# Performance work log

Hardware: AMD Instinct MI355X
Metric: run time of the kernel (lower is better)

Reference implementation:

```python
import jax, jax.numpy as jnp
import numpy as np

B, C, W, H, D = 2, 256, 32, 32, 32
CH = C // 2  # 128
LN_EPS = 1e-5


def _spatial_pool(x, wm, bm):
    # x: [B,C,W,H,D]; wm: [C]; bm: scalar. 1x1x1 conv C->1 == channel dot.
    b, c = x.shape[0], x.shape[1]
    xf = x.reshape(b, c, -1)                       # [B,C,N]
    mask = jnp.einsum('bcn,c->bn', xf, wm) + bm    # [B,N]
    attn = jax.nn.softmax(mask, axis=1)            # softmax over spatial N
    return jnp.einsum('bcn,bn->bc', xf, attn)      # [B,C] weighted-sum pool


def _channel_add(ctx, w1, b1, g, be, w2, b2):
    # 1x1 conv C->C/2, LayerNorm over C/2, ReLU, 1x1 conv C/2->C
    h = ctx @ w1.T + b1                            # [B,CH]
    mu = jnp.mean(h, axis=-1, keepdims=True)
    var = jnp.mean((h - mu) ** 2, axis=-1, keepdims=True)
    h = (h - mu) * jax.lax.rsqrt(var + LN_EPS) * g + be
    h = jax.nn.relu(h)
    return h @ w2.T + b2                           # [B,C]


def setup_inputs() -> dict:
    key = jax.random.key(0)
    ks = jax.random.split(key, 20)
    s = 0.02
    d = {
        'preds_S': jax.random.normal(ks[0], (B, C, W, H, D), jnp.float32),
        'preds_T': jax.random.normal(ks[1], (B, C, W, H, D), jnp.float32),
        'wm_s': jax.random.normal(ks[2], (C,), jnp.float32) * s,
        'bm_s': jnp.zeros((), jnp.float32),
        'wm_t': jax.random.normal(ks[3], (C,), jnp.float32) * s,
        'bm_t': jnp.zeros((), jnp.float32),
        'w1_s': jax.random.normal(ks[4], (CH, C), jnp.float32) * s,
        'b1_s': jnp.zeros((CH,), jnp.float32),
        'g_s': jnp.ones((CH,), jnp.float32),
        'be_s': jnp.zeros((CH,), jnp.float32),
        'w2_s': jax.random.normal(ks[5], (C, CH), jnp.float32) * s,
        'b2_s': jnp.zeros((C,), jnp.float32),
        'w1_t': jax.random.normal(ks[6], (CH, C), jnp.float32) * s,
        'b1_t': jnp.zeros((CH,), jnp.float32),
        'g_t': jnp.ones((CH,), jnp.float32),
        'be_t': jnp.zeros((CH,), jnp.float32),
        'w2_t': jax.random.normal(ks[7], (C, CH), jnp.float32) * s,
        'b2_t': jnp.zeros((C,), jnp.float32),
    }
    return d


def reference(preds_S, preds_T, wm_s, bm_s, wm_t, bm_t,
              w1_s, b1_s, g_s, be_s, w2_s, b2_s,
              w1_t, b1_t, g_t, be_t, w2_t, b2_t):
    ctx_s = _spatial_pool(preds_S, wm_s, bm_s)     # [B,C]
    ctx_t = _spatial_pool(preds_T, wm_t, bm_t)
    add_s = _channel_add(ctx_s, w1_s, b1_s, g_s, be_s, w2_s, b2_s)  # [B,C]
    add_t = _channel_add(ctx_t, w1_t, b1_t, g_t, be_t, w2_t, b2_t)
    out_s = preds_S + add_s[:, :, None, None, None]
    out_t = preds_T + add_t[:, :, None, None, None]
    diff = out_s - out_t
    return jnp.sum(diff * diff) / preds_S.shape[0]
```

## Files before the change

### kernel.cpp

```cpp
#include <hip/hip_runtime.h>
#include <math.h>

#define Bc   2
#define Cc   256
#define Nn   32768
#define CHc  128
#define LN_EPS 1e-5f

#define TN    64
#define TPB   512
#define NQ    16
#define CG    32
#define CPG   8
#define GRIDX (Nn / TN)

__global__ __launch_bounds__(TPB, 2) void gc_fused(
    const float* __restrict__ S, const float* __restrict__ T,
    const float* __restrict__ wms, const float* __restrict__ bms,
    const float* __restrict__ wmt, const float* __restrict__ bmt,
    float* __restrict__ ctxnum,
    float* __restrict__ rowsum,
    float* __restrict__ den,
    float* __restrict__ sumsq) {
  const int b    = blockIdx.y;
  const int tid  = threadIdx.x;
  const int nq   = tid & (NQ - 1);
  const int cg   = tid >> 4;
  const int wv   = tid >> 6;
  const int lane = tid & 63;
  const int c0   = cg * CPG;
  const int n0   = blockIdx.x * TN + nq * 4;

  __shared__ float4 mredw[2][8][NQ];
  __shared__ float  cred[Cc * 17];
  __shared__ float  sqred[8];
  __shared__ float  denred[2][NQ];

  const float bS = bms[0];
  const float bT = bmt[0];

  const float* Sp = S + ((size_t)b * Cc + c0) * Nn + n0;
  const float* Tp = T + ((size_t)b * Cc + c0) * Nn + n0;

  float4 s4[CPG], t4[CPG];
#pragma unroll
  for (int i = 0; i < CPG; ++i) s4[i] = *(const float4*)(Sp + (size_t)i * Nn);
#pragma unroll
  for (int i = 0; i < CPG; ++i) t4[i] = *(const float4*)(Tp + (size_t)i * Nn);

  float wS[CPG], wT[CPG];
#pragma unroll
  for (int i = 0; i < CPG; ++i) { wS[i] = wms[c0 + i]; wT[i] = wmt[c0 + i]; }

  float4 ms = make_float4(0.f, 0.f, 0.f, 0.f);
  float4 mt = make_float4(0.f, 0.f, 0.f, 0.f);
#pragma unroll
  for (int i = 0; i < CPG; ++i) {
    ms.x += wS[i] * s4[i].x; ms.y += wS[i] * s4[i].y;
    ms.z += wS[i] * s4[i].z; ms.w += wS[i] * s4[i].w;
    mt.x += wT[i] * t4[i].x; mt.y += wT[i] * t4[i].y;
    mt.z += wT[i] * t4[i].z; mt.w += wT[i] * t4[i].w;
  }

#pragma unroll
  for (int m = 16; m <= 32; m <<= 1) {
    ms.x += __shfl_xor(ms.x, m); ms.y += __shfl_xor(ms.y, m);
    ms.z += __shfl_xor(ms.z, m); ms.w += __shfl_xor(ms.w, m);
    mt.x += __shfl_xor(mt.x, m); mt.y += __shfl_xor(mt.y, m);
    mt.z += __shfl_xor(mt.z, m); mt.w += __shfl_xor(mt.w, m);
  }
  if (lane < NQ) { mredw[0][wv][nq] = ms; mredw[1][wv][nq] = mt; }

  __syncthreads();

  float4 Ms = make_float4(0.f, 0.f, 0.f, 0.f);
  float4 Mt = make_float4(0.f, 0.f, 0.f, 0.f);
#pragma unroll
  for (int w = 0; w < 8; ++w) {
    const float4 a = mredw[0][w][nq];
    Ms.x += a.x; Ms.y += a.y; Ms.z += a.z; Ms.w += a.w;
    const float4 c = mredw[1][w][nq];
    Mt.x += c.x; Mt.y += c.y; Mt.z += c.z; Mt.w += c.w;
  }
  float4 es, et;
  es.x = __expf(Ms.x + bS); es.y = __expf(Ms.y + bS);
  es.z = __expf(Ms.z + bS); es.w = __expf(Ms.w + bS);
  et.x = __expf(Mt.x + bT); et.y = __expf(Mt.y + bT);
  et.z = __expf(Mt.z + bT); et.w = __expf(Mt.w + bT);

  if (tid < NQ) {
    denred[0][tid] = es.x + es.y + es.z + es.w;
    denred[1][tid] = et.x + et.y + et.z + et.w;
  }

#pragma unroll
  for (int i = 0; i < CPG; ++i)
    cred[(c0 + i) * 17 + nq] =
        s4[i].x * es.x + s4[i].y * es.y + s4[i].z * es.z + s4[i].w * es.w;
  __syncthreads();
  if (tid < Cc) {
    float a = 0.f;
#pragma unroll
    for (int k = 0; k < NQ; ++k) a += cred[tid * 17 + k];
    atomicAdd(&ctxnum[((size_t)0 * Bc + b) * Cc + tid], a);
  } else if (tid == Cc + 1) {
    float a = 0.f, c = 0.f;
#pragma unroll
    for (int k = 0; k < NQ; ++k) { a += denred[0][k]; c += denred[1][k]; }
    atomicAdd(&den[0 * Bc + b], a);
    atomicAdd(&den[1 * Bc + b], c);
  }
  __syncthreads();

#pragma unroll
  for (int i = 0; i < CPG; ++i)
    cred[(c0 + i) * 17 + nq] =
        t4[i].x * et.x + t4[i].y * et.y + t4[i].z * et.z + t4[i].w * et.w;
  __syncthreads();
  if (tid < Cc) {
    float c = 0.f;
#pragma unroll
    for (int k = 0; k < NQ; ++k) c += cred[tid * 17 + k];
    atomicAdd(&ctxnum[((size_t)1 * Bc + b) * Cc + tid], c);
  }
  __syncthreads();

  float sq = 0.f;
#pragma unroll
  for (int i = 0; i < CPG; ++i) {
    const float dx = s4[i].x - t4[i].x, dy = s4[i].y - t4[i].y;
    const float dz = s4[i].z - t4[i].z, dw = s4[i].w - t4[i].w;
    cred[(c0 + i) * 17 + nq] = dx + dy + dz + dw;
    sq += dx * dx + dy * dy + dz * dz + dw * dw;
  }
#pragma unroll
  for (int m = 1; m < 64; m <<= 1) sq += __shfl_xor(sq, m);
  if (lane == 0) sqred[wv] = sq;
  __syncthreads();
  if (tid < Cc) {
    float r = 0.f;
#pragma unroll
    for (int k = 0; k < NQ; ++k) r += cred[tid * 17 + k];
    atomicAdd(&rowsum[(size_t)b * Cc + tid], r);
  } else if (tid == Cc) {
    float v = 0.f;
#pragma unroll
    for (int w = 0; w < 8; ++w) v += sqred[w];
    atomicAdd(sumsq, v);
  }
}

__global__ __launch_bounds__(1024) void gc_k4a_mlp(
    const float* __restrict__ ctxr, const float* __restrict__ den,
    const float* __restrict__ w1s, const float* __restrict__ b1s,
    const float* __restrict__ gs,  const float* __restrict__ bes,
    const float* __restrict__ w2s, const float* __restrict__ b2s,
    const float* __restrict__ w1t, const float* __restrict__ b1t,
    const float* __restrict__ gt,  const float* __restrict__ bet,
    const float* __restrict__ w2t, const float* __restrict__ b2t,
    float* __restrict__ addv) {
  const int tt  = blockIdx.x >> 1;
  const int b   = blockIdx.x & 1;
  const int tid = threadIdx.x;

  const float* w1 = tt ? w1t : w1s;
  const float* b1 = tt ? b1t : b1s;
  const float* g  = tt ? gt  : gs;
  const float* be = tt ? bet : bes;
  const float* w2 = tt ? w2t : w2s;
  const float* b2 = tt ? b2t : b2s;

  __shared__ float cxs[Cc];
  __shared__ float part[1024];
  __shared__ float hbuf[CHc];
  __shared__ float hr[CHc];
  __shared__ float2 red2[128];
  __shared__ float mu_s, rstd_s;

  if (tid < Cc)
    cxs[tid] = ctxr[((size_t)tt * Bc + b) * Cc + tid] / den[tt * Bc + b];
  __syncthreads();

  {
    const int j = tid >> 3, s = tid & 7;
    const float* wr = w1 + j * Cc + s * 32;
    const float4* cx4 = (const float4*)(cxs + s * 32);
    float acc = 0.f;
#pragma unroll
    for (int k = 0; k < 8; ++k) {
      const float4 w = *(const float4*)(wr + k * 4);
      const float4 x = cx4[k];
      acc += w.x * x.x + w.y * x.y + w.z * x.z + w.w * x.w;
    }
    part[tid] = acc;
  }
  __syncthreads();
  if (tid < CHc) {
    float h = b1[tid];
#pragma unroll
    for (int q = 0; q < 8; ++q) h += part[tid * 8 + q];
    hbuf[tid] = h;
  }
  __syncthreads();

  if (tid < CHc) {
    const float v = hbuf[tid];
    red2[tid] = make_float2(v, v * v);
  }
  __syncthreads();
  for (int s = 64; s > 0; s >>= 1) {
    if (tid < s) {
      red2[tid].x += red2[tid + s].x;
      red2[tid].y += red2[tid + s].y;
    }
    __syncthreads();
  }
  if (tid == 0) {
    const float mu = red2[0].x / (float)CHc;
    const float var = red2[0].y / (float)CHc - mu * mu;
    mu_s = mu;
    rstd_s = rsqrtf(var + LN_EPS);
  }
  __syncthreads();
  if (tid < CHc) {
    const float v = (hbuf[tid] - mu_s) * rstd_s * g[tid] + be[tid];
    hr[tid] = v > 0.f ? v : 0.f;
  }
  __syncthreads();

  {
    const int c = tid >> 2, q = tid & 3;
    const float* wr = w2 + c * CHc + q * 32;
    const float4* h4 = (const float4*)(hr + q * 32);
    float acc = 0.f;
#pragma unroll
    for (int k = 0; k < 8; ++k) {
      const float4 w = *(const float4*)(wr + k * 4);
      const float4 x = h4[k];
      acc += w.x * x.x + w.y * x.y + w.z * x.z + w.w * x.w;
    }
    part[tid] = acc;
  }
  __syncthreads();
  if (tid < Cc) {
    float acc = b2[tid];
#pragma unroll
    for (int q = 0; q < 4; ++q) acc += part[tid * 4 + q];
    addv[((size_t)tt * Bc + b) * Cc + tid] = acc;
  }
}

__global__ __launch_bounds__(256) void gc_k4b_final(
    const float* __restrict__ addv, const float* __restrict__ rowsum,
    const float* __restrict__ sumsq, float* __restrict__ out) {
  const int tid = threadIdx.x;
  __shared__ float red[256];
  float part = 0.f;
  for (int job = tid; job < Bc * Cc; job += 256) {
    const int c = job & (Cc - 1);
    const int b = job >> 8;
    const float delta = addv[((size_t)0 * Bc + b) * Cc + c] -
                        addv[((size_t)1 * Bc + b) * Cc + c];
    part += 2.f * delta * rowsum[(size_t)b * Cc + c] +
            (float)Nn * delta * delta;
  }
  red[tid] = part;
  __syncthreads();
  for (int s = 128; s > 0; s >>= 1) {
    if (tid < s) red[tid] += red[tid + s];
    __syncthreads();
  }
  if (tid == 0) out[0] = (red[0] + sumsq[0]) / (float)Bc;
}

extern "C" void kernel_launch(void* const* d_in, const int* in_sizes, int n_in,
                              void* d_out, int out_size, void* d_ws,
                              size_t ws_size, hipStream_t stream) {
  const float* S   = (const float*)d_in[0];
  const float* T   = (const float*)d_in[1];
  const float* wms = (const float*)d_in[2];
  const float* bms = (const float*)d_in[3];
  const float* wmt = (const float*)d_in[4];
  const float* bmt = (const float*)d_in[5];
  const float* w1s = (const float*)d_in[6];
  const float* b1s = (const float*)d_in[7];
  const float* gs  = (const float*)d_in[8];
  const float* bes = (const float*)d_in[9];
  const float* w2s = (const float*)d_in[10];
  const float* b2s = (const float*)d_in[11];
  const float* w1t = (const float*)d_in[12];
  const float* b1t = (const float*)d_in[13];
  const float* gt  = (const float*)d_in[14];
  const float* bet = (const float*)d_in[15];
  const float* w2t = (const float*)d_in[16];
  const float* b2t = (const float*)d_in[17];
  float* out = (float*)d_out;

  float* ws     = (float*)d_ws;
  float* ctxnum = ws;
  float* rowsum = ctxnum + 2 * Bc * Cc;
  float* den    = rowsum + Bc * Cc;
  float* sumsq  = den + 4;
  float* addv   = sumsq + 1;

  hipMemsetAsync(d_ws, 0, (2 * Bc * Cc + Bc * Cc + 4 + 1) * sizeof(float),
                 stream);

  gc_fused<<<dim3(GRIDX, Bc), TPB, 0, stream>>>(S, T, wms, bms, wmt, bmt,
                                                ctxnum, rowsum, den, sumsq);
  gc_k4a_mlp<<<4, 1024, 0, stream>>>(ctxnum, den, w1s, b1s, gs, bes, w2s, b2s,
                                     w1t, b1t, gt, bet, w2t, b2t, addv);
  gc_k4b_final<<<1, 256, 0, stream>>>(addv, rowsum, sumsq, out);
}
```

Before: 205.8 us.

## Merge shared-memory reductions into one barrier and fuse final kernel via last-block atomic

The fused streaming kernel gets three separate shared-memory scratch arrays, one each for the S-weighted, T-weighted and difference partials. This replaces four barrier-separated reduction phases with a single barrier, and the work is split so the upper 256 threads reduce the T context in parallel with the lower 256. Empty asm constraints pin the loaded S/T values in registers. The final scalar reduction kernel is folded into the MLP kernel through a last-block-done atomic counter, removing one launch. In exchange, shared memory rises from about 17KB to about 52KB per block, which may lower occupancy at two blocks per CU.

```diff
diff --git a/kernel.cpp b/kernel.cpp
--- a/kernel.cpp
+++ b/kernel.cpp
@@ -32,7 +32,9 @@
   const int n0   = blockIdx.x * TN + nq * 4;
 
   __shared__ float4 mredw[2][8][NQ];
-  __shared__ float  cred[Cc * 17];
+  __shared__ float  creds[Cc * 17];
+  __shared__ float  credt[Cc * 17];
+  __shared__ float  credd[Cc * 17];
   __shared__ float  sqred[8];
   __shared__ float  denred[2][NQ];
 
@@ -63,6 +65,14 @@
   }
 
 #pragma unroll
+  for (int i = 0; i < CPG; ++i) {
+    asm volatile("" : "+v"(s4[i].x), "+v"(s4[i].y), "+v"(s4[i].z),
+                      "+v"(s4[i].w));
+    asm volatile("" : "+v"(t4[i].x), "+v"(t4[i].y), "+v"(t4[i].z),
+                      "+v"(t4[i].w));
+  }
+
+#pragma unroll
   for (int m = 16; m <= 32; m <<= 1) {
     ms.x += __shfl_xor(ms.x, m); ms.y += __shfl_xor(ms.y, m);
     ms.z += __shfl_xor(ms.z, m); ms.w += __shfl_xor(ms.w, m);
@@ -95,62 +105,57 @@
 
 #pragma unroll
   for (int i = 0; i < CPG; ++i)
-    cred[(c0 + i) * 17 + nq] =
+    creds[(c0 + i) * 17 + nq] =
         s4[i].x * es.x + s4[i].y * es.y + s4[i].z * es.z + s4[i].w * es.w;
-  __syncthreads();
-  if (tid < Cc) {
-    float a = 0.f;
-#pragma unroll
-    for (int k = 0; k < NQ; ++k) a += cred[tid * 17 + k];
-    atomicAdd(&ctxnum[((size_t)0 * Bc + b) * Cc + tid], a);
-  } else if (tid == Cc + 1) {
-    float a = 0.f, c = 0.f;
-#pragma unroll
-    for (int k = 0; k < NQ; ++k) { a += denred[0][k]; c += denred[1][k]; }
-    atomicAdd(&den[0 * Bc + b], a);
-    atomicAdd(&den[1 * Bc + b], c);
-  }
-  __syncthreads();
-
 #pragma unroll
   for (int i = 0; i < CPG; ++i)
-    cred[(c0 + i) * 17 + nq] =
+    credt[(c0 + i) * 17 + nq] =
         t4[i].x * et.x + t4[i].y * et.y + t4[i].z * et.z + t4[i].w * et.w;
-  __syncthreads();
-  if (tid < Cc) {
-    float c = 0.f;
-#pragma unroll
-    for (int k = 0; k < NQ; ++k) c += cred[tid * 17 + k];
-    atomicAdd(&ctxnum[((size_t)1 * Bc + b) * Cc + tid], c);
-  }
-  __syncthreads();
 
   float sq = 0.f;
 #pragma unroll
   for (int i = 0; i < CPG; ++i) {
     const float dx = s4[i].x - t4[i].x, dy = s4[i].y - t4[i].y;
     const float dz = s4[i].z - t4[i].z, dw = s4[i].w - t4[i].w;
-    cred[(c0 + i) * 17 + nq] = dx + dy + dz + dw;
+    credd[(c0 + i) * 17 + nq] = dx + dy + dz + dw;
     sq += dx * dx + dy * dy + dz * dz + dw * dw;
   }
 #pragma unroll
   for (int m = 1; m < 64; m <<= 1) sq += __shfl_xor(sq, m);
   if (lane == 0) sqred[wv] = sq;
-  __syncthreads();
+
+  __syncthreads();
+
   if (tid < Cc) {
-    float r = 0.f;
-#pragma unroll
-    for (int k = 0; k < NQ; ++k) r += cred[tid * 17 + k];
+    float a = 0.f, r = 0.f;
+#pragma unroll
+    for (int k = 0; k < NQ; ++k) a += creds[tid * 17 + k];
+#pragma unroll
+    for (int k = 0; k < NQ; ++k) r += credd[tid * 17 + k];
+    atomicAdd(&ctxnum[((size_t)0 * Bc + b) * Cc + tid], a);
     atomicAdd(&rowsum[(size_t)b * Cc + tid], r);
-  } else if (tid == Cc) {
-    float v = 0.f;
-#pragma unroll
-    for (int w = 0; w < 8; ++w) v += sqred[w];
-    atomicAdd(sumsq, v);
+  } else {
+    const int c = tid - Cc;
+    float t = 0.f;
+#pragma unroll
+    for (int k = 0; k < NQ; ++k) t += credt[c * 17 + k];
+    atomicAdd(&ctxnum[((size_t)1 * Bc + b) * Cc + c], t);
+    if (tid == Cc) {
+      float v = 0.f;
+#pragma unroll
+      for (int w = 0; w < 8; ++w) v += sqred[w];
+      atomicAdd(sumsq, v);
+    } else if (tid == Cc + 1) {
+      float a = 0.f, cden = 0.f;
+#pragma unroll
+      for (int k = 0; k < NQ; ++k) { a += denred[0][k]; cden += denred[1][k]; }
+      atomicAdd(&den[0 * Bc + b], a);
+      atomicAdd(&den[1 * Bc + b], cden);
+    }
   }
 }
 
-__global__ __launch_bounds__(1024) void gc_k4a_mlp(
+__global__ __launch_bounds__(1024) void gc_k4_mlp_final(
     const float* __restrict__ ctxr, const float* __restrict__ den,
     const float* __restrict__ w1s, const float* __restrict__ b1s,
     const float* __restrict__ gs,  const float* __restrict__ bes,
@@ -158,7 +163,9 @@
     const float* __restrict__ w1t, const float* __restrict__ b1t,
     const float* __restrict__ gt,  const float* __restrict__ bet,
     const float* __restrict__ w2t, const float* __restrict__ b2t,
-    float* __restrict__ addv) {
+    const float* __restrict__ rowsum, const float* __restrict__ sumsq,
+    float* __restrict__ addv, unsigned int* __restrict__ bump,
+    float* __restrict__ out) {
   const int tt  = blockIdx.x >> 1;
   const int b   = blockIdx.x & 1;
   const int tid = threadIdx.x;
@@ -176,6 +183,8 @@
   __shared__ float hr[CHc];
   __shared__ float2 red2[128];
   __shared__ float mu_s, rstd_s;
+  __shared__ unsigned int lastv;
+  __shared__ float red[256];
 
   if (tid < Cc)
     cxs[tid] = ctxr[((size_t)tt * Bc + b) * Cc + tid] / den[tt * Bc + b];
@@ -248,29 +257,32 @@
     for (int q = 0; q < 4; ++q) acc += part[tid * 4 + q];
     addv[((size_t)tt * Bc + b) * Cc + tid] = acc;
   }
-}
-
-__global__ __launch_bounds__(256) void gc_k4b_final(
-    const float* __restrict__ addv, const float* __restrict__ rowsum,
-    const float* __restrict__ sumsq, float* __restrict__ out) {
-  const int tid = threadIdx.x;
-  __shared__ float red[256];
-  float part = 0.f;
-  for (int job = tid; job < Bc * Cc; job += 256) {
-    const int c = job & (Cc - 1);
-    const int b = job >> 8;
-    const float delta = addv[((size_t)0 * Bc + b) * Cc + c] -
-                        addv[((size_t)1 * Bc + b) * Cc + c];
-    part += 2.f * delta * rowsum[(size_t)b * Cc + c] +
-            (float)Nn * delta * delta;
-  }
-  red[tid] = part;
-  __syncthreads();
-  for (int s = 128; s > 0; s >>= 1) {
-    if (tid < s) red[tid] += red[tid + s];
+
+  __threadfence();
+  __syncthreads();
+  if (tid == 0) lastv = atomicAdd(bump, 1u);
+  __syncthreads();
+  if (lastv == 3u) {
+    __threadfence();
+    float p = 0.f;
+    if (tid < 256) {
+      for (int job = tid; job < Bc * Cc; job += 256) {
+        const int c = job & (Cc - 1);
+        const int bb = job >> 8;
+        const float delta = addv[((size_t)0 * Bc + bb) * Cc + c] -
+                            addv[((size_t)1 * Bc + bb) * Cc + c];
+        p += 2.f * delta * rowsum[(size_t)bb * Cc + c] +
+             (float)Nn * delta * delta;
+      }
+      red[tid] = p;
+    }
     __syncthreads();
-  }
-  if (tid == 0) out[0] = (red[0] + sumsq[0]) / (float)Bc;
+    for (int s = 128; s > 0; s >>= 1) {
+      if (tid < s) red[tid] += red[tid + s];
+      __syncthreads();
+    }
+    if (tid == 0) out[0] = (red[0] + sumsq[0]) / (float)Bc;
+  }
 }
 
 extern "C" void kernel_launch(void* const* d_in, const int* in_sizes, int n_in,
@@ -301,14 +313,16 @@
   float* rowsum = ctxnum + 2 * Bc * Cc;
   float* den    = rowsum + Bc * Cc;
   float* sumsq  = den + 4;
-  float* addv   = sumsq + 1;
-
-  hipMemsetAsync(d_ws, 0, (2 * Bc * Cc + Bc * Cc + 4 + 1) * sizeof(float),
-                 stream);
+  unsigned int* bump = (unsigned int*)(sumsq + 1);
+  float* addv   = (float*)(bump + 1);
+
+  hipMemsetAsync(d_ws, 0,
+                 (2 * Bc * Cc + Bc * Cc + 4 + 1 + 1) * sizeof(float), stream);
 
   gc_fused<<<dim3(GRIDX, Bc), TPB, 0, stream>>>(S, T, wms, bms, wmt, bmt,
                                                 ctxnum, rowsum, den, sumsq);
-  gc_k4a_mlp<<<4, 1024, 0, stream>>>(ctxnum, den, w1s, b1s, gs, bes, w2s, b2s,
-                                     w1t, b1t, gt, bet, w2t, b2t, addv);
-  gc_k4b_final<<<1, 256, 0, stream>>>(addv, rowsum, sumsq, out);
+  gc_k4_mlp_final<<<4, 1024, 0, stream>>>(ctxnum, den, w1s, b1s, gs, bes,
+                                          w2s, b2s, w1t, b1t, gt, bet,
+                                          w2t, b2t, rowsum, sumsq, addv,
+                                          bump, out);
 }
```

Measured after the change: 217.0 us. 1.05x slower.
